# Kernel optimization log

Hardware: AMD Instinct MI355X
Metric: run time of the kernel (lower is better)

The kernel has to match this reference:

```python
import jax, jax.numpy as jnp
import numpy as np

N, E, C, H, G, NC = 100000, 1600000, 128, 128, 256, 10
NEG_SLOPE = 0.2


def setup_inputs() -> dict:
    key = jax.random.key(0)
    ks = jax.random.split(key, 12)
    return {
        "x": jax.random.normal(ks[0], (N, C), jnp.float32),
        "edge_index": jax.random.randint(ks[1], (2, E), 0, N),
        "edge_attr": jax.random.uniform(ks[2], (E,), jnp.float32),
        "batch": jnp.sort(jax.random.randint(ks[3], (N,), 0, G)),
        "num_graphs": G,
        "att": jax.random.normal(ks[4], (3, 2 * C), jnp.float32) * (6.0 / (1 + 2 * C)) ** 0.5,
        "W1": jax.random.normal(ks[5], (3, C, H), jnp.float32) * (1.0 / C) ** 0.5,
        "b1": jnp.zeros((3, H), jnp.float32),
        "W2": jax.random.normal(ks[6], (3, H, H), jnp.float32) * (1.0 / H) ** 0.5,
        "b2": jnp.zeros((3, H), jnp.float32),
        "fc1_w": jax.random.normal(ks[7], (6 * H, 2 * H), jnp.float32) * (1.0 / (6 * H)) ** 0.5,
        "fc1_b": jnp.zeros((2 * H,), jnp.float32),
        "fc2_w": jax.random.normal(ks[8], (2 * H, H), jnp.float32) * (1.0 / (2 * H)) ** 0.5,
        "fc2_b": jnp.zeros((H,), jnp.float32),
        "fc3_w": jax.random.normal(ks[9], (H, NC), jnp.float32) * (1.0 / H) ** 0.5,
        "fc3_b": jnp.zeros((NC,), jnp.float32),
    }


def segment_sparsemax(z, seg, num_segments):
    """Exact sparsemax within each segment (ragged), vectorized via lexsort."""
    n = z.shape[0]
    order = jnp.lexsort((-z, seg))          # by segment asc, value desc
    zs, ss = z[order], seg[order]
    counts = jax.ops.segment_sum(jnp.ones((n,), jnp.int32), seg, num_segments)
    starts = jnp.cumsum(counts) - counts    # exclusive prefix -> segment start
    pos = jnp.arange(n, dtype=jnp.int32) - starts[ss]   # 0-based rank in segment
    ecs = jnp.cumsum(zs)
    base = jnp.concatenate([jnp.zeros((1,), zs.dtype), ecs])[starts[ss]]
    segcum = ecs - base                     # inclusive within-segment cumsum
    cond = 1.0 + (pos + 1).astype(zs.dtype) * zs > segcum  # support prefix mask
    k = jax.ops.segment_sum(cond.astype(zs.dtype), ss, num_segments)
    sum_k = jax.ops.segment_sum(jnp.where(cond, zs, 0.0), ss, num_segments)
    tau = jnp.where(k > 0, (sum_k - 1.0) / jnp.maximum(k, 1.0), 0.0)
    return jnp.maximum(z - tau[seg], 0.0)


def gcn_conv(x, row, col, ew, W, b, n_nodes):
    """PyG GCNConv with edge weights + self-loops (fill value 1)."""
    h = x @ W                                            # [N, H]
    deg = jax.ops.segment_sum(ew, col, n_nodes) + 1.0    # self-loop weight 1
    dinv = jnp.where(deg > 0, jax.lax.rsqrt(deg), 0.0)
    norm = dinv[row] * ew * dinv[col]                    # per-edge norm
    out = jax.ops.segment_sum(norm[:, None] * h[row], col, n_nodes)
    out = out + h * (dinv * dinv)[:, None]               # self-loop contribution
    return out + b


def emodel_block(x, row, col, att_b, W1_b, b1_b, W2_b, b2_b, n_nodes):
    # Edgelayer: att * cat([x[row], x[col]]) summed -> leaky_relu -> sparsemax(row)
    c = x.shape[1]
    s1 = x @ att_b[:c]                                   # [N]
    s2 = x @ att_b[c:]
    w = s1[row] + s2[col]
    w = jnp.where(w >= 0, w, NEG_SLOPE * w)              # leaky_relu
    p = segment_sparsemax(w, row, n_nodes)               # zero weight == pruned edge
    h = jax.nn.relu(gcn_conv(x, row, col, p, W1_b, b1_b, n_nodes))
    h = jax.nn.relu(gcn_conv(h, row, col, p, W2_b, b2_b, n_nodes))
    return h


def global_pools(z, batch, num_graphs):
    cnt = jax.ops.segment_sum(jnp.ones((z.shape[0], 1), z.dtype), batch, num_graphs)
    mean = jax.ops.segment_sum(z, batch, num_graphs) / jnp.maximum(cnt, 1.0)
    mx = jax.ops.segment_max(z, batch, num_graphs)
    mx = jnp.where(jnp.isfinite(mx), mx, 0.0)            # guard empty graphs
    return mean, mx


def reference(x, edge_index, edge_attr, batch, num_graphs, att, W1, b1, W2, b2,
              fc1_w, fc1_b, fc2_w, fc2_b, fc3_w, fc3_b):
    n_nodes = x.shape[0]
    row, col = edge_index[0], edge_index[1]
    feats = []
    for i in range(3):  # three structurally identical blocks with distinct params
        z = emodel_block(x, row, col, att[i], W1[i], b1[i], W2[i], b2[i], n_nodes)
        mean, mx = global_pools(z, batch, num_graphs)
        feats += [mean, mx]
    h = jnp.concatenate(feats, axis=1)                   # [G, 6*H]
    h = jax.nn.relu(h @ fc1_w + fc1_b)
    h = jax.nn.relu(h @ fc2_w + fc2_b)
    return jax.nn.log_softmax(h @ fc3_w + fc3_b, axis=-1)
```

## Files before the change

### kernel.cpp

```cpp
#include <hip/hip_runtime.h>
#include <math.h>

constexpr int NN   = 100000;
constexpr int EE   = 1600000;
constexpr int CH   = 128;
constexpr int GG   = 256;
constexpr int NCLS = 10;
constexpr int SW   = 48;
constexpr int QW   = 24;

constexpr int NB   = (NN + 255) >> 8;
constexpr int BCAP = 4608;
constexpr int EPT  = 8;
constexpr int BINTB = 256;
constexpr int EPB  = BINTB * EPT;

typedef _Float16 half8  __attribute__((ext_vector_type(8)));
typedef _Float16 half2v __attribute__((ext_vector_type(2)));
typedef float    float4v __attribute__((ext_vector_type(4)));

__global__ void bounds_kernel(const int* __restrict__ batch, int* __restrict__ gb,
                              int* __restrict__ bcur) {
    int t = blockIdx.x * blockDim.x + threadIdx.x;
    if (t < NB) bcur[t] = 0;
    if (t > GG) return;
    int lo = 0, hi = NN;
    while (lo < hi) {
        int mid = (lo + hi) >> 1;
        if (batch[mid] < t) lo = mid + 1; else hi = mid;
    }
    gb[t] = lo;
}

__global__ void wt16_kernel(const float* __restrict__ W1, const float* __restrict__ W2,
                            _Float16* __restrict__ wt) {
    int mat = blockIdx.x;
    const float* src = (mat < 3) ? (W1 + (size_t)mat * 16384)
                                 : (W2 + (size_t)(mat - 3) * 16384);
    _Float16* dst = wt + (size_t)mat * 16384;
    for (int i = threadIdx.x; i < 16384; i += 256) {
        int n = i >> 7, k = i & 127;
        dst[n * 128 + k] = (_Float16)src[k * 128 + n];
    }
}

__global__ void scores3_kernel(const float* __restrict__ x, const float* __restrict__ att,
                               float* __restrict__ s1, float* __restrict__ s2,
                               int* __restrict__ cur, _Float16* __restrict__ x16) {
    int wid  = threadIdx.x >> 6;
    int lane = threadIdx.x & 63;
    int node = blockIdx.x * 4 + wid;
    if (node >= NN) return;
    float x0 = x[node * CH + lane];
    float x1 = x[node * CH + 64 + lane];
    x16[(size_t)node * CH + lane]      = (_Float16)x0;
    x16[(size_t)node * CH + 64 + lane] = (_Float16)x1;
#pragma unroll
    for (int i = 0; i < 3; ++i) {
        const float* a = att + i * 256;
        float p1 = x0 * a[lane]       + x1 * a[64 + lane];
        float p2 = x0 * a[128 + lane] + x1 * a[192 + lane];
#pragma unroll
        for (int off = 32; off > 0; off >>= 1) {
            p1 += __shfl_xor(p1, off, 64);
            p2 += __shfl_xor(p2, off, 64);
        }
        if (lane == 0) { s1[i * NN + node] = p1; s2[i * NN + node] = p2; }
    }
    if (lane == 0) {
        cur[node]          = 0;
        cur[NN + node]     = 0;
        cur[2 * NN + node] = 0;
    }
}

__global__ __launch_bounds__(256) void bin_kernel(const int* __restrict__ ei,
                                                  int* __restrict__ bcur,
                                                  unsigned int* __restrict__ binned) {
    __shared__ int hist[NB];
    __shared__ int basearr[NB];
    int tid = threadIdx.x;
    for (int b = tid; b < NB; b += BINTB) hist[b] = 0;
    __syncthreads();
    int e0 = blockIdx.x * EPB;
    int r[EPT], c[EPT], off[EPT];
#pragma unroll
    for (int j = 0; j < EPT; ++j) {
        int e = e0 + j * BINTB + tid;
        if (e < EE) {
            r[j] = ei[e];
            c[j] = ei[EE + e];
            off[j] = atomicAdd(&hist[r[j] >> 8], 1);
        } else r[j] = -1;
    }
    __syncthreads();
    for (int b = tid; b < NB; b += BINTB) {
        int n = hist[b];
        basearr[b] = n ? atomicAdd(&bcur[b], n) : 0;
    }
    __syncthreads();
#pragma unroll
    for (int j = 0; j < EPT; ++j) {
        if (r[j] >= 0) {
            int b = r[j] >> 8;
            int pos = basearr[b] + off[j];
            if (pos < BCAP)
                binned[(size_t)b * BCAP + pos] = (unsigned)(r[j] & 255) | ((unsigned)c[j] << 8);
        }
    }
}

__global__ __launch_bounds__(1024) void buildtau_kernel(const int* __restrict__ bcur,
                                                        const unsigned int* __restrict__ binned,
                                                        const float* __restrict__ s1,
                                                        const float* __restrict__ s2,
                                                        float* __restrict__ taubuf) {
    __shared__ int slot[256 * SW];
    __shared__ int cntl[256];
    int b   = blockIdx.x;
    int tid = threadIdx.x;
    for (int i = tid; i < 256; i += 1024) cntl[i] = 0;
    __syncthreads();
    int cnt = min(bcur[b], BCAP);
    for (int idx = tid; idx < cnt; idx += 1024) {
        unsigned u = binned[(size_t)b * BCAP + idx];
        int rlo = u & 255;
        int p = atomicAdd(&cntl[rlo], 1);
        if (p < SW) slot[rlo * SW + p] = (int)(u >> 8);
    }
    __syncthreads();
    int wid  = tid >> 6, lane = tid & 63;
    int half = lane >> 5, l32 = lane & 31;
    const float NEGINF = __int_as_float(0xff800000);
    for (int pp = 0; pp < 8; ++pp) {
        int pb = wid * 16 + pp * 2;
        int v0 = (b << 8) + pb;
        if (v0 >= NN) break;
        int d0 = min(cntl[pb], SW), d1 = min(cntl[pb + 1], SW);
        if ((d0 | d1) == 0) continue;
        if (d0 <= 32 && d1 <= 32) {
            int mydeg = half ? d1 : d0;
            int myrlo = pb + half;
            int vv    = v0 + half;
            int c = (l32 < mydeg) ? slot[myrlo * SW + l32] : 0;
#pragma unroll
            for (int i = 0; i < 3; ++i) {
                float z = NEGINF;
                if (l32 < mydeg) {
                    float w = s1[i * NN + vv] + s2[i * NN + c];
                    z = (w >= 0.f) ? w : 0.2f * w;
                }
#pragma unroll
                for (int k = 2; k <= 32; k <<= 1) {
#pragma unroll
                    for (int j = k >> 1; j > 0; j >>= 1) {
                        float other = __shfl_xor(z, j, 64);
                        bool keepMax = ((l32 & j) == 0) == ((l32 & k) == 0);
                        z = keepMax ? fmaxf(z, other) : fminf(z, other);
                    }
                }
                float cs = z;
#pragma unroll
                for (int off = 1; off < 32; off <<= 1) {
                    float t = __shfl_up(cs, off, 64);
                    if (l32 >= off) cs += t;
                }
                bool cond = (l32 < mydeg) && (1.f + (float)(l32 + 1) * z > cs);
                unsigned long long m = __ballot(cond);
                int myk = half ? __popcll(m >> 32) : __popcll(m & 0xFFFFFFFFull);
                float sumk = __shfl(cs, half * 32 + max(myk, 1) - 1, 64);
                if (l32 == 0 && mydeg > 0)
                    taubuf[i * NN + vv] = (sumk - 1.f) / (float)max(myk, 1);
            }
        } else {
            for (int h = 0; h < 2; ++h) {
                int deg = h ? d1 : d0;
                if (deg == 0) continue;
                int rlo = pb + h;
                int v   = v0 + h;
                int c = (lane < deg) ? slot[rlo * SW + lane] : 0;
#pragma unroll
                for (int i = 0; i < 3; ++i) {
                    float z = NEGINF;
                    if (lane < deg) {
                        float w = s1[i * NN + v] + s2[i * NN + c];
                        z = (w >= 0.f) ? w : 0.2f * w;
                    }
#pragma unroll
                    for (int k = 2; k <= 64; k <<= 1) {
#pragma unroll
                        for (int j = k >> 1; j > 0; j >>= 1) {
                            float other = __shfl_xor(z, j, 64);
                            bool keepMax = ((lane & j) == 0) == ((lane & k) == 0);
                            z = keepMax ? fmaxf(z, other) : fminf(z, other);
                        }
                    }
                    float cs = z;
#pragma unroll
                    for (int off = 1; off < 64; off <<= 1) {
                        float t = __shfl_up(cs, off, 64);
                        if (lane >= off) cs += t;
                    }
                    bool cond = (lane < deg) && (1.f + (float)(lane + 1) * z > cs);
                    unsigned long long mask = __ballot(cond);
                    int k = __popcll(mask);
                    float sumk = __shfl(cs, k - 1, 64);
                    if (lane == 0) taubuf[i * NN + v] = (sumk - 1.f) / (float)k;
                }
            }
        }
    }
}

__global__ void compact_kernel(const int* __restrict__ ei, const float* __restrict__ s1,
                               const float* __restrict__ s2, const float* __restrict__ taubuf,
                               int* __restrict__ qcnt, int2* __restrict__ qslot) {
    int e = blockIdx.x * blockDim.x + threadIdx.x;
    if (e >= EE) return;
    int r = ei[e], c = ei[EE + e];
    float w = s1[r] + s2[c];
    w = (w >= 0.f) ? w : 0.2f * w;
    float p = w - taubuf[r];
    if (p > 0.f) {
        int pos = atomicAdd(&qcnt[c], 1);
        if (pos < QW) qslot[c * QW + pos] = make_int2(r, __float_as_int(p));
    }
}

__global__ void degq_kernel(const int* __restrict__ qcnt, const int2* __restrict__ qslot,
                            float* __restrict__ dinv) {
    int v = blockIdx.x * blockDim.x + threadIdx.x;
    if (v >= NN) return;
    int cnt = min(qcnt[v], QW);
    double d = 1.0;
    int base = v * QW;
    for (int t = 0; t < cnt; ++t) d += (double)__int_as_float(qslot[base + t].y);
    dinv[v] = rsqrtf((float)d);
}

__global__ __launch_bounds__(256) void gemm16_kernel(const _Float16* __restrict__ A,
                                                     const _Float16* __restrict__ WT,
                                                     _Float16* __restrict__ Cout, int M) {
    int lane = threadIdx.x & 63;
    int wid  = threadIdx.x >> 6;
    int l15  = lane & 15;
    int quad = lane >> 4;
    int rowbase = blockIdx.x * 64 + wid * 16;
    int arow = rowbase + l15;

    float4v acc[8];
#pragma unroll
    for (int n = 0; n < 8; ++n) acc[n] = (float4v){0.f, 0.f, 0.f, 0.f};

#pragma unroll
    for (int kc = 0; kc < 4; ++kc) {
        half8 a = {};
        if (arow < M) a = *(const half8*)(A + (size_t)arow * CH + kc * 32 + quad * 8);
#pragma unroll
        for (int n = 0; n < 8; ++n) {
            half8 b = *(const half8*)(WT + (size_t)(n * 16 + l15) * CH + kc * 32 + quad * 8);
            acc[n] = __builtin_amdgcn_mfma_f32_16x16x32_f16(a, b, acc[n], 0, 0, 0);
        }
    }
#pragma unroll
    for (int n = 0; n < 8; ++n) {
#pragma unroll
        for (int r = 0; r < 4; ++r) {
            int row = rowbase + quad * 4 + r;
            if (row < M) Cout[(size_t)row * CH + n * 16 + l15] = (_Float16)acc[n][r];
        }
    }
}

template <int OUTMODE>
__global__ void agg_kernel(const _Float16* __restrict__ hin,
                           const int* __restrict__ qcnt, const int2* __restrict__ qslot,
                           const float* __restrict__ dinv, const float* __restrict__ bias,
                           void* __restrict__ outv) {
    int wid  = threadIdx.x >> 6;
    int lane = threadIdx.x & 63;
    int v = blockIdx.x * 4 + wid;
    if (v >= NN) return;
    const half2v* hin2 = (const half2v*)hin;
    int cnt  = min(qcnt[v], QW);
    int base = v * QW;
    float dv = dinv[v];
    double ax = 0.0, ay = 0.0;
    for (int t = 0; t < cnt; ++t) {
        int2 ep = qslot[base + t];
        int r = ep.x;
        float g = __int_as_float(ep.y) * dinv[r];
        half2v hr = hin2[(size_t)r * 64 + lane];
        ax += (double)g * (double)(float)hr.x;
        ay += (double)g * (double)(float)hr.y;
    }
    half2v hv = hin2[(size_t)v * 64 + lane];
    float2 b2 = ((const float2*)bias)[lane];
    float ox = fmaxf(dv * (float)ax + dv * dv * (float)hv.x + b2.x, 0.f);
    float oy = fmaxf(dv * (float)ay + dv * dv * (float)hv.y + b2.y, 0.f);
    if (OUTMODE == 0) {
        half2v o; o.x = (_Float16)ox; o.y = (_Float16)oy;
        ((half2v*)outv)[(size_t)v * 64 + lane] = o;
    } else {
        float2 o; o.x = ox; o.y = oy;
        ((float2*)outv)[(size_t)v * 64 + lane] = o;
    }
}

__global__ void pool_kernel(const float* __restrict__ z, const int* __restrict__ gb,
                            float* __restrict__ feats, int blk) {
    int g = blockIdx.x;
    int f = threadIdx.x;
    int s = gb[g], e = gb[g + 1];
    float sum = 0.f, mx = 0.f;
    const float* zp = z + (size_t)s * CH + f;
    int n = s;
    for (; n + 16 <= e; n += 16) {
        float v[16];
#pragma unroll
        for (int j = 0; j < 16; ++j) v[j] = zp[(size_t)j * CH];
#pragma unroll
        for (int j = 0; j < 16; ++j) {
            sum += v[j];
            mx = fmaxf(mx, v[j]);
        }
        zp += (size_t)16 * CH;
    }
    for (; n < e; ++n) {
        float v = *zp;
        sum += v;
        mx = fmaxf(mx, v);
        zp += CH;
    }
    int cnt = e - s;
    feats[g * 768 + blk * 256 + f]       = sum / (float)max(cnt, 1);
    feats[g * 768 + blk * 256 + 128 + f] = mx;
}

__global__ void fc1_kernel(const float* __restrict__ feats, const float* __restrict__ w,
                           const float* __restrict__ b, float* __restrict__ t1) {
    __shared__ float lf[768];
    int g = blockIdx.x, j = threadIdx.x;
    for (int i = j; i < 768; i += 256) lf[i] = feats[g * 768 + i];
    __syncthreads();
    float acc = b[j];
    for (int k = 0; k < 768; ++k) acc += lf[k] * w[k * 256 + j];
    t1[g * 256 + j] = fmaxf(acc, 0.f);
}

__global__ void fc23_kernel(const float* __restrict__ t1,
                            const float* __restrict__ w2, const float* __restrict__ b2,
                            const float* __restrict__ w3, const float* __restrict__ b3,
                            float* __restrict__ out) {
    __shared__ float lt[256];
    __shared__ float lh[128];
    __shared__ float lg[NCLS];
    int g = blockIdx.x, j = threadIdx.x;
    lt[j]       = t1[g * 256 + j];
    lt[j + 128] = t1[g * 256 + 128 + j];
    __syncthreads();
    float acc = b2[j];
    for (int k = 0; k < 256; ++k) acc += lt[k] * w2[k * 128 + j];
    lh[j] = fmaxf(acc, 0.f);
    __syncthreads();
    if (j < NCLS) {
        float a = b3[j];
        for (int k = 0; k < 128; ++k) a += lh[k] * w3[k * NCLS + j];
        lg[j] = a;
    }
    __syncthreads();
    if (j == 0) {
        float mxv = lg[0];
        for (int i = 1; i < NCLS; ++i) mxv = fmaxf(mxv, lg[i]);
        float se = 0.f;
        for (int i = 0; i < NCLS; ++i) se += expf(lg[i] - mxv);
        float lse = logf(se) + mxv;
        for (int i = 0; i < NCLS; ++i) out[g * NCLS + i] = lg[i] - lse;
    }
}

extern "C" void kernel_launch(void* const* d_in, const int* in_sizes, int n_in,
                              void* d_out, int out_size, void* d_ws, size_t ws_size,
                              hipStream_t stream) {
    const float* x     = (const float*)d_in[0];
    const int*   ei    = (const int*)  d_in[1];
    const int*   batch = (const int*)  d_in[3];
    const float* att   = (const float*)d_in[5];
    const float* W1    = (const float*)d_in[6];
    const float* b1    = (const float*)d_in[7];
    const float* W2    = (const float*)d_in[8];
    const float* b2    = (const float*)d_in[9];
    const float* fc1w  = (const float*)d_in[10];
    const float* fc1b  = (const float*)d_in[11];
    const float* fc2w  = (const float*)d_in[12];
    const float* fc2b  = (const float*)d_in[13];
    const float* fc3w  = (const float*)d_in[14];
    const float* fc3b  = (const float*)d_in[15];
    float* out = (float*)d_out;

    char* p = (char*)d_ws;
    auto carve = [&](size_t bytes) -> void* {
        void* r = (void*)p;
        p += (bytes + 255) & ~(size_t)255;
        return r;
    };
    int* cur  = (int*)carve((size_t)3 * NN * 4);
    int* qcnt = cur;
    void* adj = carve((size_t)NN * QW * 8);
    unsigned int* binned = (unsigned int*)adj;
    int2*         qslot  = (int2*)adj;
    int* gb   = (int*)carve((size_t)(GG + 1) * 4);
    int* bcur = (int*)carve((size_t)NB * 4);
    float* s1     = (float*)carve((size_t)3 * NN * 4);
    float* s2     = (float*)carve((size_t)3 * NN * 4);
    float* taubuf = (float*)carve((size_t)3 * NN * 4);
    float* dinv   = (float*)carve((size_t)NN * 4);
    _Float16* wt16 = (_Float16*)carve((size_t)6 * 16384 * 2);
    _Float16* x16  = (_Float16*)carve((size_t)NN * CH * 2);
    _Float16* bufA = (_Float16*)carve((size_t)NN * CH * 2);
    float* zbuf = (float*)carve((size_t)NN * CH * 4);
    _Float16* bufB = (_Float16*)zbuf;
    float* feats  = (float*)carve((size_t)GG * 768 * 4);
    float* t1     = (float*)carve((size_t)GG * 256 * 4);

    const int TB = 256;
    dim3 egrid((EE + TB - 1) / TB);
    dim3 ngrid((NN + TB - 1) / TB);
    dim3 wgrid((NN + 3) / 4);
    dim3 ggrid((NN + 63) / 64);
    dim3 bingrid((EE + EPB - 1) / EPB);

    scores3_kernel<<<wgrid, 256, 0, stream>>>(x, att, s1, s2, cur, x16);
    bounds_kernel<<<2, 256, 0, stream>>>(batch, gb, bcur);
    bin_kernel<<<bingrid, BINTB, 0, stream>>>(ei, bcur, binned);
    wt16_kernel<<<6, 256, 0, stream>>>(W1, W2, wt16);
    buildtau_kernel<<<NB, 1024, 0, stream>>>(bcur, binned, s1, s2, taubuf);

    for (int i = 0; i < 3; ++i) {
        const float* s1_i  = s1 + (size_t)i * NN;
        const float* s2_i  = s2 + (size_t)i * NN;
        const float* tau_i = taubuf + (size_t)i * NN;
        int*         qc_i  = qcnt + (size_t)i * NN;
        const _Float16* WT1_i = wt16 + (size_t)i * 16384;
        const _Float16* WT2_i = wt16 + (size_t)(3 + i) * 16384;
        const float* b1_i  = b1 + i * CH;
        const float* b2_i  = b2 + i * CH;

        compact_kernel<<<egrid, TB, 0, stream>>>(ei, s1_i, s2_i, tau_i, qc_i, qslot);
        degq_kernel<<<ngrid, TB, 0, stream>>>(qc_i, qslot, dinv);

        gemm16_kernel<<<ggrid, 256, 0, stream>>>(x16, WT1_i, bufA, NN);
        agg_kernel<0><<<wgrid, 256, 0, stream>>>(bufA, qc_i, qslot, dinv, b1_i, bufB);
        gemm16_kernel<<<ggrid, 256, 0, stream>>>(bufB, WT2_i, bufA, NN);
        agg_kernel<1><<<wgrid, 256, 0, stream>>>(bufA, qc_i, qslot, dinv, b2_i, zbuf);

        pool_kernel<<<GG, 128, 0, stream>>>(zbuf, gb, feats, i);
    }

    fc1_kernel<<<GG, 256, 0, stream>>>(feats, fc1w, fc1b, t1);
    fc23_kernel<<<GG, 128, 0, stream>>>(t1, fc2w, fc2b, fc3w, fc3b, out);
}
```

Baseline: 974.6 us.

## Shrink row bins to 64 nodes, batch sparsemax sorts, unroll low-degree aggregation

Bins edges by groups of 64 destination rows instead of 256, giving four times as many buildtau blocks with smaller shared-memory slot arrays, for more parallelism and occupancy. The bounds kernel grid grows so it can still clear all bin counters. The buildtau fast path interleaves the three bitonic sorts and prefix scans to expose instruction-level parallelism across shuffles. The aggregation kernel gets an unrolled path for up to six neighbours that issues all gathers before accumulating, which raises register use and adds redundant loads for low-degree rows.

Result: no change. 987.4 us (+1.3%).

```diff
diff --git a/kernel.cpp b/kernel.cpp
--- a/kernel.cpp
+++ b/kernel.cpp
@@ -9,8 +9,8 @@
 constexpr int SW   = 48;
 constexpr int QW   = 24;
 
-constexpr int NB   = (NN + 255) >> 8;
-constexpr int BCAP = 4608;
+constexpr int NB   = (NN + 63) >> 6;
+constexpr int BCAP = 1344;
 constexpr int EPT  = 8;
 constexpr int BINTB = 256;
 constexpr int EPB  = BINTB * EPT;
@@ -90,7 +90,7 @@
         if (e < EE) {
             r[j] = ei[e];
             c[j] = ei[EE + e];
-            off[j] = atomicAdd(&hist[r[j] >> 8], 1);
+            off[j] = atomicAdd(&hist[r[j] >> 6], 1);
         } else r[j] = -1;
     }
     __syncthreads();
@@ -102,10 +102,10 @@
 #pragma unroll
     for (int j = 0; j < EPT; ++j) {
         if (r[j] >= 0) {
-            int b = r[j] >> 8;
+            int b = r[j] >> 6;
             int pos = basearr[b] + off[j];
             if (pos < BCAP)
-                binned[(size_t)b * BCAP + pos] = (unsigned)(r[j] & 255) | ((unsigned)c[j] << 8);
+                binned[(size_t)b * BCAP + pos] = (unsigned)(r[j] & 63) | ((unsigned)c[j] << 6);
         }
     }
 }
@@ -115,26 +115,26 @@
                                                         const float* __restrict__ s1,
                                                         const float* __restrict__ s2,
                                                         float* __restrict__ taubuf) {
-    __shared__ int slot[256 * SW];
-    __shared__ int cntl[256];
+    __shared__ int slot[64 * SW];
+    __shared__ int cntl[64];
     int b   = blockIdx.x;
     int tid = threadIdx.x;
-    for (int i = tid; i < 256; i += 1024) cntl[i] = 0;
+    if (tid < 64) cntl[tid] = 0;
     __syncthreads();
     int cnt = min(bcur[b], BCAP);
     for (int idx = tid; idx < cnt; idx += 1024) {
         unsigned u = binned[(size_t)b * BCAP + idx];
-        int rlo = u & 255;
+        int rlo = u & 63;
         int p = atomicAdd(&cntl[rlo], 1);
-        if (p < SW) slot[rlo * SW + p] = (int)(u >> 8);
+        if (p < SW) slot[rlo * SW + p] = (int)(u >> 6);
     }
     __syncthreads();
     int wid  = tid >> 6, lane = tid & 63;
     int half = lane >> 5, l32 = lane & 31;
     const float NEGINF = __int_as_float(0xff800000);
-    for (int pp = 0; pp < 8; ++pp) {
-        int pb = wid * 16 + pp * 2;
-        int v0 = (b << 8) + pb;
+    for (int pp = 0; pp < 2; ++pp) {
+        int pb = wid * 4 + pp * 2;
+        int v0 = (b << 6) + pb;
         if (v0 >= NN) break;
         int d0 = min(cntl[pb], SW), d1 = min(cntl[pb + 1], SW);
         if ((d0 | d1) == 0) continue;
@@ -143,32 +143,44 @@
             int myrlo = pb + half;
             int vv    = v0 + half;
             int c = (l32 < mydeg) ? slot[myrlo * SW + l32] : 0;
+            float z[3];
 #pragma unroll
             for (int i = 0; i < 3; ++i) {
-                float z = NEGINF;
+                z[i] = NEGINF;
                 if (l32 < mydeg) {
                     float w = s1[i * NN + vv] + s2[i * NN + c];
-                    z = (w >= 0.f) ? w : 0.2f * w;
+                    z[i] = (w >= 0.f) ? w : 0.2f * w;
                 }
-#pragma unroll
-                for (int k = 2; k <= 32; k <<= 1) {
-#pragma unroll
-                    for (int j = k >> 1; j > 0; j >>= 1) {
-                        float other = __shfl_xor(z, j, 64);
-                        bool keepMax = ((l32 & j) == 0) == ((l32 & k) == 0);
-                        z = keepMax ? fmaxf(z, other) : fminf(z, other);
+            }
+#pragma unroll
+            for (int k = 2; k <= 32; k <<= 1) {
+#pragma unroll
+                for (int j = k >> 1; j > 0; j >>= 1) {
+                    bool keepMax = ((l32 & j) == 0) == ((l32 & k) == 0);
+#pragma unroll
+                    for (int i = 0; i < 3; ++i) {
+                        float other = __shfl_xor(z[i], j, 64);
+                        z[i] = keepMax ? fmaxf(z[i], other) : fminf(z[i], other);
                     }
                 }
-                float cs = z;
-#pragma unroll
-                for (int off = 1; off < 32; off <<= 1) {
-                    float t = __shfl_up(cs, off, 64);
-                    if (l32 >= off) cs += t;
+            }
+            float cs[3];
+#pragma unroll
+            for (int i = 0; i < 3; ++i) cs[i] = z[i];
+#pragma unroll
+            for (int off = 1; off < 32; off <<= 1) {
+#pragma unroll
+                for (int i = 0; i < 3; ++i) {
+                    float t = __shfl_up(cs[i], off, 64);
+                    if (l32 >= off) cs[i] += t;
                 }
-                bool cond = (l32 < mydeg) && (1.f + (float)(l32 + 1) * z > cs);
+            }
+#pragma unroll
+            for (int i = 0; i < 3; ++i) {
+                bool cond = (l32 < mydeg) && (1.f + (float)(l32 + 1) * z[i] > cs[i]);
                 unsigned long long m = __ballot(cond);
                 int myk = half ? __popcll(m >> 32) : __popcll(m & 0xFFFFFFFFull);
-                float sumk = __shfl(cs, half * 32 + max(myk, 1) - 1, 64);
+                float sumk = __shfl(cs[i], half * 32 + max(myk, 1) - 1, 64);
                 if (l32 == 0 && mydeg > 0)
                     taubuf[i * NN + vv] = (sumk - 1.f) / (float)max(myk, 1);
             }
@@ -286,13 +298,31 @@
     int base = v * QW;
     float dv = dinv[v];
     double ax = 0.0, ay = 0.0;
-    for (int t = 0; t < cnt; ++t) {
-        int2 ep = qslot[base + t];
-        int r = ep.x;
-        float g = __int_as_float(ep.y) * dinv[r];
-        half2v hr = hin2[(size_t)r * 64 + lane];
-        ax += (double)g * (double)(float)hr.x;
-        ay += (double)g * (double)(float)hr.y;
+    if (cnt > 0 && cnt <= 6) {
+        int2   ep_[6];
+        float  g_[6];
+        half2v hr_[6];
+#pragma unroll
+        for (int t = 0; t < 6; ++t) ep_[t] = qslot[base + min(t, cnt - 1)];
+#pragma unroll
+        for (int t = 0; t < 6; ++t) {
+            g_[t]  = (t < cnt) ? __int_as_float(ep_[t].y) * dinv[ep_[t].x] : 0.f;
+            hr_[t] = hin2[(size_t)ep_[t].x * 64 + lane];
+        }
+#pragma unroll
+        for (int t = 0; t < 6; ++t) {
+            ax += (double)g_[t] * (double)(float)hr_[t].x;
+            ay += (double)g_[t] * (double)(float)hr_[t].y;
+        }
+    } else {
+        for (int t = 0; t < cnt; ++t) {
+            int2 ep = qslot[base + t];
+            int r = ep.x;
+            float g = __int_as_float(ep.y) * dinv[r];
+            half2v hr = hin2[(size_t)r * 64 + lane];
+            ax += (double)g * (double)(float)hr.x;
+            ay += (double)g * (double)(float)hr.y;
+        }
     }
     half2v hv = hin2[(size_t)v * 64 + lane];
     float2 b2 = ((const float2*)bias)[lane];
@@ -429,9 +459,10 @@
     dim3 wgrid((NN + 3) / 4);
     dim3 ggrid((NN + 63) / 64);
     dim3 bingrid((EE + EPB - 1) / EPB);
+    dim3 bgrid((NB + TB - 1) / TB);
 
     scores3_kernel<<<wgrid, 256, 0, stream>>>(x, att, s1, s2, cur, x16);
-    bounds_kernel<<<2, 256, 0, stream>>>(batch, gb, bcur);
+    bounds_kernel<<<bgrid, TB, 0, stream>>>(batch, gb, bcur);
     bin_kernel<<<bingrid, BINTB, 0, stream>>>(ei, bcur, binned);
     wt16_kernel<<<6, 256, 0, stream>>>(W1, W2, wt16);
     buildtau_kernel<<<NB, 1024, 0, stream>>>(bcur, binned, s1, s2, taubuf);
```
